# Kernel tuning notes

Hardware: AMD Instinct MI355X
Metric: run time of the kernel (lower is better)

## Reference

```python
import jax, jax.numpy as jnp
import numpy as np

CLAMP_MIN, CLAMP_MAX = -60.0, 30.0


def setup_inputs() -> dict:
    key = jax.random.key(0)
    k1, k2, k3, k4 = jax.random.split(key, 4)
    b, n, d = 8, 4096, 512
    x = jax.random.normal(k1, (b, n, d), dtype=jnp.float32)
    pos = jax.random.normal(k2, (n - 1,), dtype=jnp.float32)
    zero = jax.random.normal(k3, (1,), dtype=jnp.float32)
    neg = jax.random.normal(k4, (n - 1,), dtype=jnp.float32)
    return {"x": x, "pos": pos, "zero": zero, "neg": neg}


def reference(x, pos, zero, neg):
    # ToepliztV2.forward with dim=1, normalize=False, use_exp=True,
    # type_num=-1, causal=False, and seq_len n == self.n (so l1=n-1, l2=0
    # and the -inf padding of pos/neg is empty).
    n = x.shape[1]
    # kernel of length 2n: [zero, pos, zero, neg], exp(clamp(.))
    a = jnp.exp(jnp.clip(jnp.concatenate([zero, pos, zero, neg]), CLAMP_MIN, CLAMP_MAX))
    # compute(): zero-padded FFT conv. x fft/ifft use ortho norm, kernel fft
    # uses default (backward) norm, matching the torch code exactly.
    y = jnp.fft.fft(x, 2 * n, axis=1, norm="ortho")          # [b, 2n, d] complex
    v = jnp.fft.fft(a)[None, :, None]                          # [1, 2n, 1] complex
    out = jnp.fft.ifft(v * y, 2 * n, axis=1, norm="ortho")[:, :n, :].real
    return out
```

## Files before the change

kernel.cpp:

```cpp
#include <hip/hip_runtime.h>
#include <hip/hip_bf16.h>
#include <stdint.h>

#define NSEQ 4096
#define DDIM 512
#define NB   8
#define FN   8192

#define PADI(i) ((i) + ((i) >> 5))

struct __align__(8) cf { float x, y; };

__device__ __forceinline__ cf cadd(cf a, cf b) { return {a.x + b.x, a.y + b.y}; }
__device__ __forceinline__ cf csub(cf a, cf b) { return {a.x - b.x, a.y - b.y}; }
__device__ __forceinline__ cf cmul(cf a, cf b) {
    return {a.x * b.x - a.y * b.y, a.x * b.y + a.y * b.x};
}
template<int DIR> __device__ __forceinline__ cf crot(cf z) {
    return DIR < 0 ? cf{z.y, -z.x} : cf{-z.y, z.x};
}

__device__ __forceinline__ unsigned short f2bf(float f) {
    union { float f; unsigned int u; } v;
    v.f = f;
    unsigned int u = v.u;
    u += 0x7FFFu + ((u >> 16) & 1u);
    return (unsigned short)(u >> 16);
}
__device__ __forceinline__ float bf2f(unsigned short u) {
    union { unsigned int i; float f; } v;
    v.i = (unsigned int)u << 16;
    return v.f;
}

template<int DIR>
__device__ __forceinline__ void fft4(cf& b0, cf& b1, cf& b2, cf& b3) {
    cf s0 = cadd(b0, b2), s1 = csub(b0, b2);
    cf s2 = cadd(b1, b3), s3 = crot<DIR>(csub(b1, b3));
    b0 = cadd(s0, s2); b1 = cadd(s1, s3);
    b2 = csub(s0, s2); b3 = csub(s1, s3);
}

template<int DIR>
__device__ __forceinline__ void dft8(cf a[8]) {
    cf e0 = a[0], e1 = a[2], e2 = a[4], e3 = a[6];
    cf o0 = a[1], o1 = a[3], o2 = a[5], o3 = a[7];
    fft4<DIR>(e0, e1, e2, e3);
    fft4<DIR>(o0, o1, o2, o3);
    const float c = 0.70710678118654752f;
    cf w1 = (DIR < 0) ? cf{c, -c} : cf{c, c};
    cf w3 = (DIR < 0) ? cf{-c, -c} : cf{-c, c};
    o1 = cmul(o1, w1);
    o2 = crot<DIR>(o2);
    o3 = cmul(o3, w3);
    a[0] = cadd(e0, o0); a[1] = cadd(e1, o1); a[2] = cadd(e2, o2); a[3] = cadd(e3, o3);
    a[4] = csub(e0, o0); a[5] = csub(e1, o1); a[6] = csub(e2, o2); a[7] = csub(e3, o3);
}

template<int DIR>
__device__ __forceinline__ void dft8_half(cf a0, cf a1, cf a2, cf a3, cf a[8]) {
    cf r2 = crot<DIR>(a2), r3 = crot<DIR>(a3);
    cf e0 = cadd(a0, a2), e1 = cadd(a0, r2), e2 = csub(a0, a2), e3 = csub(a0, r2);
    cf o0 = cadd(a1, a3), o1 = cadd(a1, r3), o2 = csub(a1, a3), o3 = csub(a1, r3);
    const float c = 0.70710678118654752f;
    cf w1 = (DIR < 0) ? cf{c, -c} : cf{c, c};
    cf w3 = (DIR < 0) ? cf{-c, -c} : cf{-c, c};
    o1 = cmul(o1, w1);
    o2 = crot<DIR>(o2);
    o3 = cmul(o3, w3);
    a[0] = cadd(e0, o0); a[1] = cadd(e1, o1); a[2] = cadd(e2, o2); a[3] = cadd(e3, o3);
    a[4] = csub(e0, o0); a[5] = csub(e1, o1); a[6] = csub(e2, o2); a[7] = csub(e3, o3);
}

__device__ __forceinline__ void twpow(cf w1, cf w[8]) {
    w[1] = w1;
    w[2] = cmul(w1, w1);
    w[3] = cmul(w[2], w1);
    w[4] = cmul(w[2], w[2]);
    w[5] = cmul(w[4], w1);
    w[6] = cmul(w[4], w[2]);
    w[7] = cmul(w[4], w[3]);
}

template<int DIR, int NTHR, int LM>
__device__ __forceinline__ void r8_stage_t(cf* Z, const cf* Wt, int tid) {
    const int m = 1 << LM;
#pragma unroll
    for (int q = 0; q < 1024 / NTHR; ++q) {
        int beta = q * NTHR + tid;
        int j = beta & (m - 1);
        int g = beta >> LM;
        int base = (g << (LM + 3)) + j;
        cf a[8];
#pragma unroll
        for (int r = 0; r < 8; ++r) a[r] = Z[PADI(base + (r << LM))];
        cf w1 = Wt[j << (10 - LM)];
        if (DIR > 0) w1.y = -w1.y;
        cf w[8];
        twpow(w1, w);
        if (DIR > 0) {
#pragma unroll
            for (int k = 1; k < 8; ++k) a[k] = cmul(a[k], w[k]);
        }
        dft8<DIR>(a);
        if (DIR < 0) {
#pragma unroll
            for (int k = 1; k < 8; ++k) a[k] = cmul(a[k], w[k]);
        }
#pragma unroll
        for (int r = 0; r < 8; ++r) Z[PADI(base + (r << LM))] = a[r];
    }
}

template<int NTHR>
__device__ __forceinline__ void r2_stage(cf* Z, int tid) {
#pragma unroll
    for (int q = 0; q < 4096 / NTHR; ++q) {
        int beta = q * NTHR + tid;
        int i0 = PADI(2 * beta), i1 = i0 + 1;
        cf a = Z[i0], b = Z[i1];
        Z[i0] = cadd(a, b);
        Z[i1] = csub(a, b);
    }
}

template<int DIR, int NTHR>
__device__ __forceinline__ void r8_stage(cf* Z, int lm, int tid) {
    const int m = 1 << lm;
    const float ang0 = ((DIR < 0) ? -6.2831853071795865f : 6.2831853071795865f)
                       / (float)(m * 8);
#pragma unroll
    for (int q = 0; q < 1024 / NTHR; ++q) {
        int beta = q * NTHR + tid;
        int j = beta & (m - 1);
        int g = beta >> lm;
        int base = (g << (lm + 3)) + j;
        cf a[8];
#pragma unroll
        for (int r = 0; r < 8; ++r) a[r] = Z[PADI(base + (r << lm))];
        float sn, cs;
        __sincosf(ang0 * (float)j, &sn, &cs);
        cf w[8];
        twpow({cs, sn}, w);
        if (DIR > 0) {
#pragma unroll
            for (int k = 1; k < 8; ++k) a[k] = cmul(a[k], w[k]);
        }
        dft8<DIR>(a);
        if (DIR < 0) {
#pragma unroll
            for (int k = 1; k < 8; ++k) a[k] = cmul(a[k], w[k]);
        }
#pragma unroll
        for (int r = 0; r < 8; ++r) Z[PADI(base + (r << lm))] = a[r];
    }
}

__global__ void transpose_x(const float* __restrict__ x,
                            unsigned short* __restrict__ xT) {
    __shared__ unsigned short tl[64][72];
    int t   = blockIdx.x;
    int b   = t >> 9;
    int rem = t & 511;
    int j0  = (rem >> 3) << 6;
    int d0  = (rem & 7) << 6;
    const float* xb = x + (size_t)b * NSEQ * DDIM;
#pragma unroll
    for (int e = 0; e < 4; ++e) {
        int idx = e * 256 + threadIdx.x;
        int r   = idx >> 4;
        int c4  = (idx & 15) << 2;
        float4 v = *(const float4*)&xb[(size_t)(j0 + r) * DDIM + d0 + c4];
        ushort4 o;
        o.x = f2bf(v.x); o.y = f2bf(v.y); o.z = f2bf(v.z); o.w = f2bf(v.w);
        *(ushort4*)&tl[r][c4] = o;
    }
    __syncthreads();
    unsigned short* xtb = xT + (size_t)b * DDIM * NSEQ;
#pragma unroll
    for (int e = 0; e < 4; ++e) {
        int idx = e * 256 + threadIdx.x;
        int d   = idx >> 4;
        int jq  = (idx & 15) << 2;
        ushort4 o;
        o.x = tl[jq + 0][d]; o.y = tl[jq + 1][d];
        o.z = tl[jq + 2][d]; o.w = tl[jq + 3][d];
        *(ushort4*)&xtb[(size_t)(d0 + d) * NSEQ + j0 + jq] = o;
    }
}

__global__ __launch_bounds__(512) void build_V(const float* __restrict__ pos,
                                               const float* __restrict__ zero,
                                               const float* __restrict__ neg,
                                               cf* __restrict__ Vh) {
    __shared__ cf Z[PADI(FN)];
    int tid = threadIdx.x;
    float zv = zero[0];
#pragma unroll
    for (int q = 0; q < 16; ++q) {
        int t = q * 512 + tid;
        float v;
        if (t == 0 || t == NSEQ) v = zv;
        else if (t < NSEQ)       v = pos[t - 1];
        else                     v = neg[t - NSEQ - 1];
        v = fminf(fmaxf(v, -60.0f), 30.0f);
        Z[PADI(t)] = {__expf(v), 0.0f};
    }
    __syncthreads();
    r8_stage<-1, 512>(Z, 10, tid); __syncthreads();
    r8_stage<-1, 512>(Z, 7,  tid); __syncthreads();
    r8_stage<-1, 512>(Z, 4,  tid); __syncthreads();
    r8_stage<-1, 512>(Z, 1,  tid); __syncthreads();
    r2_stage<512>(Z, tid);         __syncthreads();
    const float sc = 1.0f / (float)FN;
#pragma unroll
    for (int q = 0; q < 16; ++q) {
        int i = q * 512 + tid;
        cf v = Z[PADI(i)];
        Vh[i] = {v.x * sc, v.y * sc};
    }
}

__global__ __launch_bounds__(512, 4) void fft_conv(unsigned short* __restrict__ xT,
                                                   const cf* __restrict__ Vh) {
    __shared__ cf Z[PADI(FN)];
    __shared__ cf Wt[1024];
    int tid = threadIdx.x;
    int blk = blockIdx.x;
    int b   = blk >> 8;
    int dp  = blk & 255;
    unsigned short* col0 = xT + ((size_t)(b * DDIM + 2 * dp)) * NSEQ;
    unsigned short* col1 = col0 + NSEQ;

#pragma unroll
    for (int q = 0; q < 2; ++q) {
        int t = q * 512 + tid;
        float sn, cs;
        __sincosf(-7.66990393942820625e-04f * (float)t, &sn, &cs);
        Wt[t] = {cs, sn};
    }
    __syncthreads();

#pragma unroll
    for (int q = 0; q < 2; ++q) {
        int j = q * 512 + tid;
        cf a0 = {bf2f(col0[j]),        bf2f(col1[j])};
        cf a1 = {bf2f(col0[j + 1024]), bf2f(col1[j + 1024])};
        cf a2 = {bf2f(col0[j + 2048]), bf2f(col1[j + 2048])};
        cf a3 = {bf2f(col0[j + 3072]), bf2f(col1[j + 3072])};
        cf a[8];
        dft8_half<-1>(a0, a1, a2, a3, a);
        cf w[8];
        twpow(Wt[j], w);
#pragma unroll
        for (int k = 1; k < 8; ++k) a[k] = cmul(a[k], w[k]);
#pragma unroll
        for (int r = 0; r < 8; ++r) Z[PADI(j + (r << 10))] = a[r];
    }
    __syncthreads();

    r8_stage_t<-1, 512, 7>(Z, Wt, tid);  __syncthreads();
    r8_stage_t<-1, 512, 4>(Z, Wt, tid);  __syncthreads();

    const float4* V4 = (const float4*)Vh;
#pragma unroll
    for (int q = 0; q < 2; ++q) {
        const int idx = q * 512 + tid;
        const int g  = idx >> 1;
        const int jj = idx & 1;
        const int base = g * 16 + jj;
        cf a[8];
#pragma unroll
        for (int r = 0; r < 8; ++r) a[r] = Z[PADI(base + 2 * r)];
        dft8<-1>(a);
        const float C1 = 0.92387953251128674f, S1 = 0.38268343236508977f;
        const float C2 = 0.70710678118654752f;
        if (jj) {
            a[1] = cmul(a[1], {C1, -S1});
            a[2] = cmul(a[2], {C2, -C2});
            a[3] = cmul(a[3], {S1, -C1});
            a[4] = crot<-1>(a[4]);
            a[5] = cmul(a[5], {-S1, -C1});
            a[6] = cmul(a[6], {-C2, -C2});
            a[7] = cmul(a[7], {-C1, -S1});
        }
#pragma unroll
        for (int r = 0; r < 8; ++r) {
            cf own = a[r];
            cf oth;
            oth.x = __shfl_xor(own.x, 1);
            oth.y = __shfl_xor(own.y, 1);
            float4 v = V4[g * 8 + r];
            cf V0 = {v.x, v.y}, V1 = {v.z, v.w};
            cf Vp = cadd(V0, V1), Vm = csub(V0, V1);
            a[r] = cadd(cmul(Vp, own), cmul(Vm, oth));
        }
        if (jj) {
            a[1] = cmul(a[1], {C1, S1});
            a[2] = cmul(a[2], {C2, C2});
            a[3] = cmul(a[3], {S1, C1});
            a[4] = crot<1>(a[4]);
            a[5] = cmul(a[5], {-S1, C1});
            a[6] = cmul(a[6], {-C2, C2});
            a[7] = cmul(a[7], {-C1, S1});
        }
        dft8<1>(a);
#pragma unroll
        for (int r = 0; r < 8; ++r) Z[PADI(base + 2 * r)] = a[r];
    }
    __syncthreads();

    r8_stage_t<1, 512, 4>(Z, Wt, tid);   __syncthreads();
    r8_stage_t<1, 512, 7>(Z, Wt, tid);   __syncthreads();

#pragma unroll
    for (int q = 0; q < 2; ++q) {
        int j = q * 512 + tid;
        cf a[8];
#pragma unroll
        for (int r = 0; r < 8; ++r) a[r] = Z[PADI(j + (r << 10))];
        cf w1 = Wt[j];
        w1.y = -w1.y;
        cf w[8];
        twpow(w1, w);
#pragma unroll
        for (int k = 1; k < 8; ++k) a[k] = cmul(a[k], w[k]);
        dft8<1>(a);
#pragma unroll
        for (int r = 0; r < 4; ++r) {
            col0[j + (r << 10)] = f2bf(a[r].x);
            col1[j + (r << 10)] = f2bf(a[r].y);
        }
    }
}

__global__ void untranspose(const unsigned short* __restrict__ oT,
                            float* __restrict__ out) {
    __shared__ unsigned short tl[64][65];
    int j0 = blockIdx.x * 64, d0 = blockIdx.y * 64, b = blockIdx.z;
    const unsigned short* src = oT + (size_t)b * DDIM * NSEQ;
#pragma unroll
    for (int e = 0; e < 16; ++e) {
        int idx = e * 256 + threadIdx.x;
        int r = idx >> 6, c = idx & 63;
        tl[r][c] = src[(size_t)(d0 + r) * NSEQ + j0 + c];
    }
    __syncthreads();
    float* dst = out + ((size_t)b * NSEQ + j0) * DDIM + d0;
#pragma unroll
    for (int e = 0; e < 16; ++e) {
        int idx = e * 256 + threadIdx.x;
        int r = idx >> 6, c = idx & 63;
        dst[(size_t)r * DDIM + c] = bf2f(tl[c][r]);
    }
}

extern "C" void kernel_launch(void* const* d_in, const int* in_sizes, int n_in,
                              void* d_out, int out_size, void* d_ws, size_t ws_size,
                              hipStream_t stream) {
    const float* x    = (const float*)d_in[0];
    const float* pos  = (const float*)d_in[1];
    const float* zero = (const float*)d_in[2];
    const float* neg  = (const float*)d_in[3];
    float* out = (float*)d_out;

    unsigned short* xT = (unsigned short*)d_ws;
    cf* Vh = (cf*)((char*)d_ws + (size_t)32 * 1024 * 1024);

    build_V<<<dim3(1), 512, 0, stream>>>(pos, zero, neg, Vh);
    transpose_x<<<dim3(4096), 256, 0, stream>>>(x, xT);
    fft_conv<<<dim3(NB * 256), 512, 0, stream>>>(xT, Vh);
    untranspose<<<dim3(64, 8, 8), 256, 0, stream>>>(xT, out);
}
```

Before: 116.6 us.

## Merge kernel-spectrum build into transpose launch and vectorize complex math

Folds the single-block build_V kernel into the transpose kernel as block 0 of one launch, so the serial kernel-FFT runs alongside the transpose blocks instead of as its own launch. Transpose blocks grow to 512 threads and reuse the shared Z buffer for their tile, which makes every block reserve the large FFT-sized shared allocation and may reduce transpose occupancy. The complex type becomes a float2 ext_vector with an fma-based multiply, intended to produce packed float instructions across the FFT stages.

```diff
diff --git a/kernel.cpp b/kernel.cpp
--- a/kernel.cpp
+++ b/kernel.cpp
@@ -9,15 +9,15 @@
 
 #define PADI(i) ((i) + ((i) >> 5))
 
-struct __align__(8) cf { float x, y; };
-
-__device__ __forceinline__ cf cadd(cf a, cf b) { return {a.x + b.x, a.y + b.y}; }
-__device__ __forceinline__ cf csub(cf a, cf b) { return {a.x - b.x, a.y - b.y}; }
+typedef float cf __attribute__((ext_vector_type(2)));
+
 __device__ __forceinline__ cf cmul(cf a, cf b) {
-    return {a.x * b.x - a.y * b.y, a.x * b.y + a.y * b.x};
+    cf s = a.yx * b.yy;
+    s.x = -s.x;
+    return __builtin_elementwise_fma(a, b.xx, s);
 }
 template<int DIR> __device__ __forceinline__ cf crot(cf z) {
-    return DIR < 0 ? cf{z.y, -z.x} : cf{-z.y, z.x};
+    return DIR < 0 ? (cf){z.y, -z.x} : (cf){-z.y, z.x};
 }
 
 __device__ __forceinline__ unsigned short f2bf(float f) {
@@ -35,10 +35,10 @@
 
 template<int DIR>
 __device__ __forceinline__ void fft4(cf& b0, cf& b1, cf& b2, cf& b3) {
-    cf s0 = cadd(b0, b2), s1 = csub(b0, b2);
-    cf s2 = cadd(b1, b3), s3 = crot<DIR>(csub(b1, b3));
-    b0 = cadd(s0, s2); b1 = cadd(s1, s3);
-    b2 = csub(s0, s2); b3 = csub(s1, s3);
+    cf s0 = b0 + b2, s1 = b0 - b2;
+    cf s2 = b1 + b3, s3 = crot<DIR>(b1 - b3);
+    b0 = s0 + s2; b1 = s1 + s3;
+    b2 = s0 - s2; b3 = s1 - s3;
 }
 
 template<int DIR>
@@ -48,28 +48,28 @@
     fft4<DIR>(e0, e1, e2, e3);
     fft4<DIR>(o0, o1, o2, o3);
     const float c = 0.70710678118654752f;
-    cf w1 = (DIR < 0) ? cf{c, -c} : cf{c, c};
-    cf w3 = (DIR < 0) ? cf{-c, -c} : cf{-c, c};
+    cf w1 = (DIR < 0) ? (cf){c, -c} : (cf){c, c};
+    cf w3 = (DIR < 0) ? (cf){-c, -c} : (cf){-c, c};
     o1 = cmul(o1, w1);
     o2 = crot<DIR>(o2);
     o3 = cmul(o3, w3);
-    a[0] = cadd(e0, o0); a[1] = cadd(e1, o1); a[2] = cadd(e2, o2); a[3] = cadd(e3, o3);
-    a[4] = csub(e0, o0); a[5] = csub(e1, o1); a[6] = csub(e2, o2); a[7] = csub(e3, o3);
+    a[0] = e0 + o0; a[1] = e1 + o1; a[2] = e2 + o2; a[3] = e3 + o3;
+    a[4] = e0 - o0; a[5] = e1 - o1; a[6] = e2 - o2; a[7] = e3 - o3;
 }
 
 template<int DIR>
 __device__ __forceinline__ void dft8_half(cf a0, cf a1, cf a2, cf a3, cf a[8]) {
     cf r2 = crot<DIR>(a2), r3 = crot<DIR>(a3);
-    cf e0 = cadd(a0, a2), e1 = cadd(a0, r2), e2 = csub(a0, a2), e3 = csub(a0, r2);
-    cf o0 = cadd(a1, a3), o1 = cadd(a1, r3), o2 = csub(a1, a3), o3 = csub(a1, r3);
+    cf e0 = a0 + a2, e1 = a0 + r2, e2 = a0 - a2, e3 = a0 - r2;
+    cf o0 = a1 + a3, o1 = a1 + r3, o2 = a1 - a3, o3 = a1 - r3;
     const float c = 0.70710678118654752f;
-    cf w1 = (DIR < 0) ? cf{c, -c} : cf{c, c};
-    cf w3 = (DIR < 0) ? cf{-c, -c} : cf{-c, c};
+    cf w1 = (DIR < 0) ? (cf){c, -c} : (cf){c, c};
+    cf w3 = (DIR < 0) ? (cf){-c, -c} : (cf){-c, c};
     o1 = cmul(o1, w1);
     o2 = crot<DIR>(o2);
     o3 = cmul(o3, w3);
-    a[0] = cadd(e0, o0); a[1] = cadd(e1, o1); a[2] = cadd(e2, o2); a[3] = cadd(e3, o3);
-    a[4] = csub(e0, o0); a[5] = csub(e1, o1); a[6] = csub(e2, o2); a[7] = csub(e3, o3);
+    a[0] = e0 + o0; a[1] = e1 + o1; a[2] = e2 + o2; a[3] = e3 + o3;
+    a[4] = e0 - o0; a[5] = e1 - o1; a[6] = e2 - o2; a[7] = e3 - o3;
 }
 
 __device__ __forceinline__ void twpow(cf w1, cf w[8]) {
@@ -119,8 +119,8 @@
         int beta = q * NTHR + tid;
         int i0 = PADI(2 * beta), i1 = i0 + 1;
         cf a = Z[i0], b = Z[i1];
-        Z[i0] = cadd(a, b);
-        Z[i1] = csub(a, b);
+        Z[i0] = a + b;
+        Z[i1] = a - b;
     }
 }
 
@@ -141,7 +141,7 @@
         float sn, cs;
         __sincosf(ang0 * (float)j, &sn, &cs);
         cf w[8];
-        twpow({cs, sn}, w);
+        twpow((cf){cs, sn}, w);
         if (DIR > 0) {
 #pragma unroll
             for (int k = 1; k < 8; ++k) a[k] = cmul(a[k], w[k]);
@@ -156,68 +156,68 @@
     }
 }
 
-__global__ void transpose_x(const float* __restrict__ x,
-                            unsigned short* __restrict__ xT) {
-    __shared__ unsigned short tl[64][72];
-    int t   = blockIdx.x;
-    int b   = t >> 9;
-    int rem = t & 511;
-    int j0  = (rem >> 3) << 6;
-    int d0  = (rem & 7) << 6;
-    const float* xb = x + (size_t)b * NSEQ * DDIM;
-#pragma unroll
-    for (int e = 0; e < 4; ++e) {
-        int idx = e * 256 + threadIdx.x;
-        int r   = idx >> 4;
-        int c4  = (idx & 15) << 2;
-        float4 v = *(const float4*)&xb[(size_t)(j0 + r) * DDIM + d0 + c4];
-        ushort4 o;
-        o.x = f2bf(v.x); o.y = f2bf(v.y); o.z = f2bf(v.z); o.w = f2bf(v.w);
-        *(ushort4*)&tl[r][c4] = o;
-    }
-    __syncthreads();
-    unsigned short* xtb = xT + (size_t)b * DDIM * NSEQ;
-#pragma unroll
-    for (int e = 0; e < 4; ++e) {
-        int idx = e * 256 + threadIdx.x;
-        int d   = idx >> 4;
-        int jq  = (idx & 15) << 2;
-        ushort4 o;
-        o.x = tl[jq + 0][d]; o.y = tl[jq + 1][d];
-        o.z = tl[jq + 2][d]; o.w = tl[jq + 3][d];
-        *(ushort4*)&xtb[(size_t)(d0 + d) * NSEQ + j0 + jq] = o;
-    }
-}
-
-__global__ __launch_bounds__(512) void build_V(const float* __restrict__ pos,
-                                               const float* __restrict__ zero,
-                                               const float* __restrict__ neg,
-                                               cf* __restrict__ Vh) {
+__global__ __launch_bounds__(512) void prep(const float* __restrict__ x,
+                                            const float* __restrict__ pos,
+                                            const float* __restrict__ zero,
+                                            const float* __restrict__ neg,
+                                            unsigned short* __restrict__ xT,
+                                            cf* __restrict__ Vh) {
     __shared__ cf Z[PADI(FN)];
     int tid = threadIdx.x;
-    float zv = zero[0];
-#pragma unroll
-    for (int q = 0; q < 16; ++q) {
-        int t = q * 512 + tid;
-        float v;
-        if (t == 0 || t == NSEQ) v = zv;
-        else if (t < NSEQ)       v = pos[t - 1];
-        else                     v = neg[t - NSEQ - 1];
-        v = fminf(fmaxf(v, -60.0f), 30.0f);
-        Z[PADI(t)] = {__expf(v), 0.0f};
-    }
-    __syncthreads();
-    r8_stage<-1, 512>(Z, 10, tid); __syncthreads();
-    r8_stage<-1, 512>(Z, 7,  tid); __syncthreads();
-    r8_stage<-1, 512>(Z, 4,  tid); __syncthreads();
-    r8_stage<-1, 512>(Z, 1,  tid); __syncthreads();
-    r2_stage<512>(Z, tid);         __syncthreads();
-    const float sc = 1.0f / (float)FN;
-#pragma unroll
-    for (int q = 0; q < 16; ++q) {
-        int i = q * 512 + tid;
-        cf v = Z[PADI(i)];
-        Vh[i] = {v.x * sc, v.y * sc};
+    if (blockIdx.x == 0) {
+        float zv = zero[0];
+#pragma unroll
+        for (int q = 0; q < 16; ++q) {
+            int t = q * 512 + tid;
+            float v;
+            if (t == 0 || t == NSEQ) v = zv;
+            else if (t < NSEQ)       v = pos[t - 1];
+            else                     v = neg[t - NSEQ - 1];
+            v = fminf(fmaxf(v, -60.0f), 30.0f);
+            Z[PADI(t)] = (cf){__expf(v), 0.0f};
+        }
+        __syncthreads();
+        r8_stage<-1, 512>(Z, 10, tid); __syncthreads();
+        r8_stage<-1, 512>(Z, 7,  tid); __syncthreads();
+        r8_stage<-1, 512>(Z, 4,  tid); __syncthreads();
+        r8_stage<-1, 512>(Z, 1,  tid); __syncthreads();
+        r2_stage<512>(Z, tid);         __syncthreads();
+        const float sc = 1.0f / (float)FN;
+#pragma unroll
+        for (int q = 0; q < 16; ++q) {
+            int i = q * 512 + tid;
+            Vh[i] = Z[PADI(i)] * sc;
+        }
+    } else {
+        unsigned short (*tl)[72] = (unsigned short (*)[72])Z;
+        int t   = blockIdx.x - 1;
+        int b   = t >> 9;
+        int rem = t & 511;
+        int j0  = (rem >> 3) << 6;
+        int d0  = (rem & 7) << 6;
+        const float* xb = x + (size_t)b * NSEQ * DDIM;
+#pragma unroll
+        for (int e = 0; e < 2; ++e) {
+            int idx = e * 512 + tid;
+            int r   = idx >> 4;
+            int c4  = (idx & 15) << 2;
+            float4 v = *(const float4*)&xb[(size_t)(j0 + r) * DDIM + d0 + c4];
+            ushort4 o;
+            o.x = f2bf(v.x); o.y = f2bf(v.y); o.z = f2bf(v.z); o.w = f2bf(v.w);
+            *(ushort4*)&tl[r][c4] = o;
+        }
+        __syncthreads();
+        unsigned short* xtb = xT + (size_t)b * DDIM * NSEQ;
+#pragma unroll
+        for (int e = 0; e < 2; ++e) {
+            int idx = e * 512 + tid;
+            int d   = idx >> 4;
+            int jq  = (idx & 15) << 2;
+            ushort4 o;
+            o.x = tl[jq + 0][d]; o.y = tl[jq + 1][d];
+            o.z = tl[jq + 2][d]; o.w = tl[jq + 3][d];
+            *(ushort4*)&xtb[(size_t)(d0 + d) * NSEQ + j0 + jq] = o;
+        }
     }
 }
 
@@ -237,7 +237,7 @@
         int t = q * 512 + tid;
         float sn, cs;
         __sincosf(-7.66990393942820625e-04f * (float)t, &sn, &cs);
-        Wt[t] = {cs, sn};
+        Wt[t] = (cf){cs, sn};
     }
     __syncthreads();
 
@@ -276,13 +276,13 @@
         const float C1 = 0.92387953251128674f, S1 = 0.38268343236508977f;
         const float C2 = 0.70710678118654752f;
         if (jj) {
-            a[1] = cmul(a[1], {C1, -S1});
-            a[2] = cmul(a[2], {C2, -C2});
-            a[3] = cmul(a[3], {S1, -C1});
+            a[1] = cmul(a[1], (cf){C1, -S1});
+            a[2] = cmul(a[2], (cf){C2, -C2});
+            a[3] = cmul(a[3], (cf){S1, -C1});
             a[4] = crot<-1>(a[4]);
-            a[5] = cmul(a[5], {-S1, -C1});
-            a[6] = cmul(a[6], {-C2, -C2});
-            a[7] = cmul(a[7], {-C1, -S1});
+            a[5] = cmul(a[5], (cf){-S1, -C1});
+            a[6] = cmul(a[6], (cf){-C2, -C2});
+            a[7] = cmul(a[7], (cf){-C1, -S1});
         }
 #pragma unroll
         for (int r = 0; r < 8; ++r) {
@@ -292,17 +292,17 @@
             oth.y = __shfl_xor(own.y, 1);
             float4 v = V4[g * 8 + r];
             cf V0 = {v.x, v.y}, V1 = {v.z, v.w};
-            cf Vp = cadd(V0, V1), Vm = csub(V0, V1);
-            a[r] = cadd(cmul(Vp, own), cmul(Vm, oth));
+            cf Vp = V0 + V1, Vm = V0 - V1;
+            a[r] = cmul(Vp, own) + cmul(Vm, oth);
         }
         if (jj) {
-            a[1] = cmul(a[1], {C1, S1});
-            a[2] = cmul(a[2], {C2, C2});
-            a[3] = cmul(a[3], {S1, C1});
+            a[1] = cmul(a[1], (cf){C1, S1});
+            a[2] = cmul(a[2], (cf){C2, C2});
+            a[3] = cmul(a[3], (cf){S1, C1});
             a[4] = crot<1>(a[4]);
-            a[5] = cmul(a[5], {-S1, C1});
-            a[6] = cmul(a[6], {-C2, C2});
-            a[7] = cmul(a[7], {-C1, S1});
+            a[5] = cmul(a[5], (cf){-S1, C1});
+            a[6] = cmul(a[6], (cf){-C2, C2});
+            a[7] = cmul(a[7], (cf){-C1, S1});
         }
         dft8<1>(a);
 #pragma unroll
@@ -367,8 +367,7 @@
     unsigned short* xT = (unsigned short*)d_ws;
     cf* Vh = (cf*)((char*)d_ws + (size_t)32 * 1024 * 1024);
 
-    build_V<<<dim3(1), 512, 0, stream>>>(pos, zero, neg, Vh);
-    transpose_x<<<dim3(4096), 256, 0, stream>>>(x, xT);
+    prep<<<dim3(4097), 512, 0, stream>>>(x, pos, zero, neg, xT, Vh);
     fft_conv<<<dim3(NB * 256), 512, 0, stream>>>(xT, Vh);
     untranspose<<<dim3(64, 8, 8), 256, 0, stream>>>(xT, out);
 }
```

Measured after the change: 112.3 us. 1.04x faster.
